# Performance work log

Measured on AMD Instinct MI355X. Metric: run time of the kernel, lower is better.

## Reference

```python
import jax, jax.numpy as jnp
import numpy as np

NUM_CLASSES = 80
CONF_THRE = 0.2
NMS_THRE = 0.45
MAX_DET = 300   # fixed cap replacing torch's variable-length NMS output (padded + keep mask)
IMG = 640.0


def setup_inputs() -> dict:
    key = jax.random.key(0)
    k1, k2 = jax.random.split(key)
    pred = jax.random.uniform(k1, (32, 8400, 85), dtype=jnp.float32)
    # scale cx,cy,w,h to pixel range so IoU/NMS geometry is realistic
    pred = pred.at[..., :4].multiply(IMG)
    zone = jax.random.uniform(k2, (8, 2), dtype=jnp.float32) * IMG
    return {"prediction": pred, "zone": zone}


def _pairwise_iou(b):
    # b: [B, K, 4] in x1y1x2y2
    area = jnp.clip(b[..., 2] - b[..., 0], 0.0) * jnp.clip(b[..., 3] - b[..., 1], 0.0)
    lt = jnp.maximum(b[:, :, None, :2], b[:, None, :, :2])
    rb = jnp.minimum(b[:, :, None, 2:], b[:, None, :, 2:])
    wh = jnp.clip(rb - lt, 0.0)
    inter = wh[..., 0] * wh[..., 1]
    return inter / (area[:, :, None] + area[:, None, :] - inter + 1e-9)


def _postprocess(prediction):
    # decode cx,cy,w,h -> x1,y1,x2,y2
    xy = prediction[..., :2]
    wh = prediction[..., 2:4]
    boxes = jnp.concatenate([xy - wh * 0.5, xy + wh * 0.5], axis=-1)  # [B,N,4]
    obj = prediction[..., 4]                                           # [B,N]
    cls = prediction[..., 5:5 + NUM_CLASSES]
    class_conf = jnp.max(cls, axis=-1)                                 # [B,N]
    class_pred = jnp.argmax(cls, axis=-1)                              # [B,N]

    # confidence mask (obj * class_conf >= thre); invalid -> -inf so top_k drops them
    nms_score = obj * class_conf
    nms_score = jnp.where(nms_score >= CONF_THRE, nms_score, -jnp.inf)

    s, idx = jax.lax.top_k(nms_score, MAX_DET)                         # [B,K]
    b = jnp.take_along_axis(boxes, idx[..., None], axis=1)             # [B,K,4]

    # class-agnostic greedy NMS on score-sorted boxes (matches torchvision.ops.nms)
    iou = _pairwise_iou(b)                                             # [B,K,K]
    keep = jnp.isfinite(s)                                             # valid (passed conf) entries
    ar = jnp.arange(MAX_DET)
    def body(i, keep):
        sup = keep[:, i][:, None] & (iou[:, i, :] > NMS_THRE) & (ar > i)
        return keep & jnp.logical_not(sup)
    keep = jax.lax.fori_loop(0, MAX_DET, body, keep)

    obj_s = jnp.take_along_axis(obj, idx, axis=1)
    conf_s = jnp.take_along_axis(class_conf, idx, axis=1)
    cls_s = jnp.take_along_axis(class_pred, idx, axis=1).astype(jnp.int32)
    # extract_boxes_scores_and_classes: score = max over columns [obj, class_conf]
    scores = jnp.maximum(obj_s, conf_s)
    return b, scores, cls_s, keep


def _points_inside_zone(px, py, zone):
    # px, py: [B,K]; zone: [Z,2]. Ray-casting parity test (faithful to torch version).
    zr = jnp.roll(zone, shift=1, axis=0)
    xi, yi = zone[:, 0], zone[:, 1]
    xj, yj = zr[:, 0], zr[:, 1]
    pyb = py[..., None]  # [B,K,1] vs [Z]
    pxb = px[..., None]
    gyi = yi > pyb
    gyj = yj > pyb
    gx = (xj - xi) * (pyb - yi) / (yj - yi) + xi
    inter = (gyi != gyj) & (gx > pxb)
    return (jnp.sum(inter.astype(jnp.int32), axis=-1) % 2) > 0


def reference(prediction, zone):
    b, scores, classes, keep = _postprocess(prediction)
    cx = (b[..., 0] + b[..., 2]) * 0.5
    cy = (b[..., 1] + b[..., 3]) * 0.5
    in_zone = _points_inside_zone(cx, cy, zone) & keep
    centers_yx = jnp.stack([cy, cx], axis=-1)                          # [B,K,2]
    boxes_yxyx = jnp.stack([b[..., 1], b[..., 0], b[..., 3], b[..., 2]], axis=-1)
    return boxes_yxyx, in_zone, scores, classes, centers_yx, keep
```

## Files before the change

kernel.cpp:

```cpp
#include <hip/hip_runtime.h>
#include <stdint.h>

typedef unsigned long long ull;

#define NA 8400
#define NB 32
#define KTOP 300
#define NC 80
#define CH 33
#define WS_STRIDE 33600
#define OFF_SEL   0
#define OFF_KEEP  2400
#define OFF_MASK  2560

#define O1 38400
#define O2 48000
#define O3 57600
#define O4 67200
#define O5 86400

__global__ __launch_bounds__(256) void score_kernel(const float* __restrict__ pred,
                                                    uint32_t* __restrict__ keys) {
    __shared__ float sP[128 * 85];
    const int blk = blockIdx.x;
    const float4* g4 = (const float4*)(pred + (size_t)blk * 128 * 85);
    float4* l4 = (float4*)sP;
    for (int i = threadIdx.x; i < (128 * 85 / 4); i += 256) l4[i] = g4[i];
    __syncthreads();
    const int t = threadIdx.x;
    if (t < 128) {
        const float* p = sP + t * 85;
        float obj = p[4];
        float b0 = p[5], b1 = p[6], b2 = p[7], b3 = p[8];
        #pragma unroll
        for (int c = 4; c < NC; c += 4) {
            b0 = fmaxf(b0, p[5 + c]);
            b1 = fmaxf(b1, p[6 + c]);
            b2 = fmaxf(b2, p[7 + c]);
            b3 = fmaxf(b3, p[8 + c]);
        }
        float best = fmaxf(fmaxf(b0, b1), fmaxf(b2, b3));
        float sc = obj * best;
        uint32_t u = (sc >= 0.2f) ? (__float_as_uint(sc) | 0x80000000u) : 0x007FFFFFu;
        keys[(size_t)blk * 128 + t] = u;
    }
}

__global__ __launch_bounds__(256) void select_kernel(const uint32_t* keys, uint8_t* ws) {
    __shared__ uint32_t sKeys[8448];
    __shared__ ull sSel[KTOP];
    __shared__ ull sSorted[KTOP];
    __shared__ uint32_t sH4[1024];
    __shared__ uint32_t sScanA[256];
    __shared__ uint32_t sScanB[256];
    __shared__ uint32_t sBc[2];
    __shared__ int sCnt;

    const int b = blockIdx.x;
    const int t = threadIdx.x;
    const int wv = t >> 6;

    for (int e = t; e < NA; e += 256) sKeys[e] = keys[(size_t)b * NA + e];
    for (int e = NA + t; e < 8448; e += 256) sKeys[e] = 0u;
    if (t == 0) sCnt = 0;
    __syncthreads();

    uint32_t prefix = 0, r = KTOP;
    const int beg = t * CH;
    const int end = (beg + CH < NA) ? beg + CH : NA;
    for (int round = 0; round < 4; ++round) {
        const int shift = 24 - 8 * round;
        for (int idx = t; idx < 1024; idx += 256) sH4[idx] = 0u;
        __syncthreads();
        const uint32_t pmask = (round == 0) ? 0u : (0xFFFFFFFFu << (shift + 8));
        for (int e = beg; e < end; ++e) {
            uint32_t k = sKeys[e];
            if ((k & pmask) == (prefix & pmask))
                atomicAdd(&sH4[(wv << 8) + ((k >> shift) & 0xFFu)], 1u);
        }
        __syncthreads();
        sScanA[t] = sH4[t] + sH4[256 + t] + sH4[512 + t] + sH4[768 + t];
        __syncthreads();
        uint32_t* src = sScanA;
        uint32_t* dst = sScanB;
        for (int off = 1; off < 256; off <<= 1) {
            uint32_t v = src[t];
            if (t + off < 256) v += src[t + off];
            dst[t] = v;
            __syncthreads();
            uint32_t* tmp = src; src = dst; dst = tmp;
        }
        uint32_t S = src[t];
        uint32_t above = (t < 255) ? src[t + 1] : 0;
        if (above < r && S >= r) {
            sBc[0] = prefix | ((uint32_t)t << shift);
            sBc[1] = r - above;
        }
        __syncthreads();
        prefix = sBc[0]; r = sBc[1];
        __syncthreads();
    }
    const uint32_t kth = prefix;
    const uint32_t rem = r;
    const uint32_t cntgt = KTOP - rem;

    {
        uint32_t eqc = 0;
        for (int e = beg; e < end; ++e) {
            uint32_t k = sKeys[e];
            if (k > kth) {
                int p = atomicAdd(&sCnt, 1);
                sSel[p] = ((ull)k << 32) | (ull)(0xFFFFFFFFu - (uint32_t)e);
            } else if (k == kth) eqc++;
        }
        sScanA[t] = eqc;
        __syncthreads();
        uint32_t* src = sScanA;
        uint32_t* dst = sScanB;
        for (int off = 1; off < 256; off <<= 1) {
            uint32_t v = src[t];
            if (t >= off) v += src[t - off];
            dst[t] = v;
            __syncthreads();
            uint32_t* tmp = src; src = dst; dst = tmp;
        }
        uint32_t off0 = (t > 0) ? src[t - 1] : 0;
        for (int e = beg; e < end; ++e) {
            uint32_t k = sKeys[e];
            if (k == kth) {
                if (off0 < rem)
                    sSel[cntgt + off0] = ((ull)k << 32) | (ull)(0xFFFFFFFFu - (uint32_t)e);
                off0++;
            }
        }
        __syncthreads();
    }

    ull my0 = sSel[t];
    ull my1 = (t < KTOP - 256) ? sSel[256 + t] : 0ull;
    int r0 = 0, r1 = 0;
    for (int j = 0; j < KTOP; ++j) {
        ull v = sSel[j];
        r0 += (v > my0) ? 1 : 0;
        r1 += (v > my1) ? 1 : 0;
    }
    sSorted[r0] = my0;
    if (t < KTOP - 256) sSorted[r1] = my1;
    __syncthreads();

    ull* selW = (ull*)(ws + (size_t)b * WS_STRIDE + OFF_SEL);
    ull* keepW = (ull*)(ws + (size_t)b * WS_STRIDE + OFF_KEEP);
    bool f = ((uint32_t)(sSorted[t] >> 32)) > 0x007FFFFFu;
    ull m = __ballot(f);
    if ((t & 63) == 0) keepW[t >> 6] = m;
    if (t < 64) {
        bool f2 = (t < KTOP - 256) && (((uint32_t)(sSorted[256 + t] >> 32)) > 0x007FFFFFu);
        ull m2 = __ballot(f2);
        if (t == 0) keepW[4] = m2;
    }
    selW[t] = sSorted[t];
    if (t < KTOP - 256) selW[256 + t] = sSorted[256 + t];
}

__global__ __launch_bounds__(256) void prep_kernel(const float* __restrict__ pred,
                                                   uint8_t* ws,
                                                   float* __restrict__ out) {
    #pragma clang fp contract(off)
    __shared__ float sB0[KTOP], sB1[KTOP], sB2[KTOP], sB3[KTOP];
    const int role = blockIdx.x;
    const int b = blockIdx.y;
    const int t = threadIdx.x;
    const ull* sel = (const ull*)(ws + (size_t)b * WS_STRIDE + OFF_SEL);

    if (role < 5) {
        for (int i = t; i < KTOP; i += 256) {
            uint32_t a = 0xFFFFFFFFu - (uint32_t)sel[i];
            const float* p = pred + ((size_t)b * NA + a) * 85;
            float x = p[0], y = p[1], w = p[2], h = p[3];
            float hw = w * 0.5f, hh = h * 0.5f;
            sB0[i] = x - hw; sB1[i] = y - hh; sB2[i] = x + hw; sB3[i] = y + hh;
        }
        __syncthreads();
        ull* mask = (ull*)(ws + (size_t)b * WS_STRIDE + OFF_MASK);
        const int j0 = role * 64;
        int jmax = j0 + 64; if (jmax > KTOP) jmax = KTOP;
        for (int i = t; i < KTOP; i += 256) {
            float x1 = sB0[i], y1 = sB1[i], x2 = sB2[i], y2 = sB3[i];
            float ai = fmaxf(x2 - x1, 0.0f) * fmaxf(y2 - y1, 0.0f);
            ull bits = 0ull;
            int jbeg = (j0 > i + 1) ? j0 : (i + 1);
            for (int j = jbeg; j < jmax; ++j) {
                float bx1 = sB0[j], by1 = sB1[j], bx2 = sB2[j], by2 = sB3[j];
                float aj = fmaxf(bx2 - bx1, 0.0f) * fmaxf(by2 - by1, 0.0f);
                float iw = fminf(x2, bx2) - fmaxf(x1, bx1); iw = fmaxf(iw, 0.0f);
                float ih = fminf(y2, by2) - fmaxf(y1, by1); ih = fmaxf(ih, 0.0f);
                float inter = iw * ih;
                float den = ai + aj;
                den = den - inter;
                den = den + 1e-9f;
                float iou = inter / den;
                if (iou > 0.45f) bits |= (1ull << (j - j0));
            }
            mask[i * 5 + role] = bits;
        }
    } else {
        const size_t bo = (size_t)b * KTOP;
        for (int i = t; i < KTOP; i += 256) {
            uint32_t a = 0xFFFFFFFFu - (uint32_t)sel[i];
            const float* p = pred + ((size_t)b * NA + a) * 85;
            float x = p[0], y = p[1], w = p[2], h = p[3], obj = p[4];
            float best = p[5]; int bc = 0;
            for (int c = 1; c < NC; ++c) {
                float v = p[5 + c];
                if (v > best) { best = v; bc = c; }
            }
            float hw = w * 0.5f, hh = h * 0.5f;
            float x1 = x - hw, y1 = y - hh, x2 = x + hw, y2 = y + hh;
            out[(bo + i) * 4 + 0] = y1;
            out[(bo + i) * 4 + 1] = x1;
            out[(bo + i) * 4 + 2] = y2;
            out[(bo + i) * 4 + 3] = x2;
            out[O4 + (bo + i) * 2 + 0] = (y1 + y2) * 0.5f;
            out[O4 + (bo + i) * 2 + 1] = (x1 + x2) * 0.5f;
            out[O2 + bo + i] = fmaxf(obj, best);
            out[O3 + bo + i] = (float)bc;
        }
    }
}

__global__ __launch_bounds__(64) void finish_kernel(const float* __restrict__ zone,
                                                    const uint8_t* ws,
                                                    float* __restrict__ out) {
    #pragma clang fp contract(off)
    __shared__ float sZone[16];
    const int b = blockIdx.x;
    const int L = threadIdx.x;
    const ull* mask = (const ull*)(ws + (size_t)b * WS_STRIDE + OFF_MASK);
    const ull* keepI = (const ull*)(ws + (size_t)b * WS_STRIDE + OFF_KEEP);
    if (L < 16) sZone[L] = zone[L];

    ull rm[5][5];
    #pragma unroll
    for (int w = 0; w < 5; ++w) {
        int i = w * 64 + L;
        #pragma unroll
        for (int ww = 0; ww < 5; ++ww)
            rm[w][ww] = (i < KTOP) ? mask[i * 5 + ww] : 0ull;
    }
    ull kw[5];
    #pragma unroll
    for (int w = 0; w < 5; ++w) kw[w] = keepI[w];
    __syncthreads();

    #pragma unroll
    for (int w = 0; w < 5; ++w) {
        ull cur = kw[w];
        while (cur) {
            int ib = __builtin_ctzll(cur);
            ull m0 = __shfl(rm[w][0], ib);
            ull m1 = __shfl(rm[w][1], ib);
            ull m2 = __shfl(rm[w][2], ib);
            ull m3 = __shfl(rm[w][3], ib);
            ull m4 = __shfl(rm[w][4], ib);
            kw[0] &= ~m0; kw[1] &= ~m1; kw[2] &= ~m2; kw[3] &= ~m3; kw[4] &= ~m4;
            ull done = (ib == 63) ? 0ull : (~0ull << (ib + 1));
            cur = kw[w] & done;
        }
    }

    const size_t bo = (size_t)b * KTOP;
    #pragma unroll
    for (int h = 0; h < 5; ++h) {
        int i = h * 64 + L;
        if (i < KTOP) {
            int kp = (int)((kw[h] >> L) & 1ull);
            float cy = out[O4 + (bo + i) * 2 + 0];
            float cx = out[O4 + (bo + i) * 2 + 1];
            int cnt = 0;
            #pragma unroll
            for (int e = 0; e < 8; ++e) {
                float xi = sZone[2 * e], yi = sZone[2 * e + 1];
                int ep = (e + 7) & 7;
                float xj = sZone[2 * ep], yj = sZone[2 * ep + 1];
                bool gyi = yi > cy, gyj = yj > cy;
                if (gyi != gyj) {
                    float gx = (xj - xi) * (cy - yi) / (yj - yi) + xi;
                    if (gx > cx) cnt++;
                }
            }
            int inz = (((cnt & 1) != 0) && kp) ? 1 : 0;
            out[O1 + bo + i] = (float)inz;
            out[O5 + bo + i] = (float)kp;
        }
    }
}

extern "C" void kernel_launch(void* const* d_in, const int* in_sizes, int n_in,
                              void* d_out, int out_size, void* d_ws, size_t ws_size,
                              hipStream_t stream) {
    const float* pred = (const float*)d_in[0];
    const float* zone = (const float*)d_in[1];
    float* out = (float*)d_out;
    uint32_t* keys = (uint32_t*)d_ws;
    uint8_t* ws = (uint8_t*)d_ws;

    score_kernel<<<(NB * NA) / 128, 256, 0, stream>>>(pred, keys);
    select_kernel<<<NB, 256, 0, stream>>>(keys, ws);
    prep_kernel<<<dim3(6, NB), 256, 0, stream>>>(pred, ws, out);
    finish_kernel<<<NB, 64, 0, stream>>>(zone, ws, out);
}
```

Baseline: 203.3 us.

## Fuse select, IoU mask, NMS and zone kernels into one per-batch block

Merges the select, prep and finish kernels into a single per-batch kernel that keeps sorted selections, boxes and the IoU bitmask in a shared-memory union instead of round-tripping through global workspace. It also replaces the block-wide shared-memory scans with wavefront shuffle scans, uses 8 histogram copies instead of 4 to cut atomic contention, and overlaps the serial greedy NMS on wave 0 with output writes on the other waves. The aim is to cut launch overhead, global traffic and barrier count. In exchange, the IoU mask work that ran on 160 blocks now runs on only 32 blocks.

Result: slower. 226.6 us (+11.5%).

```diff
diff --git a/kernel.cpp b/kernel.cpp
--- a/kernel.cpp
+++ b/kernel.cpp
@@ -8,10 +8,6 @@
 #define KTOP 300
 #define NC 80
 #define CH 33
-#define WS_STRIDE 33600
-#define OFF_SEL   0
-#define OFF_KEEP  2400
-#define OFF_MASK  2560
 
 #define O1 38400
 #define O2 48000
@@ -46,22 +42,40 @@
     }
 }
 
-__global__ __launch_bounds__(256) void select_kernel(const uint32_t* keys, uint8_t* ws) {
-    __shared__ uint32_t sKeys[8448];
+__global__ __launch_bounds__(256) void batch_kernel(const float* __restrict__ pred,
+                                                    const float* __restrict__ zone,
+                                                    const uint32_t* __restrict__ keys,
+                                                    float* __restrict__ out) {
+    #pragma clang fp contract(off)
+    __shared__ union {
+        uint32_t keys[8448];
+        struct {
+            float b0[KTOP], b1[KTOP], b2[KTOP], b3[KTOP];
+            ull mask[KTOP * 5];
+        } late;
+    } u;
     __shared__ ull sSel[KTOP];
     __shared__ ull sSorted[KTOP];
-    __shared__ uint32_t sH4[1024];
-    __shared__ uint32_t sScanA[256];
-    __shared__ uint32_t sScanB[256];
+    __shared__ uint32_t sH[8 * 257];
+    __shared__ uint32_t sTot[4];
     __shared__ uint32_t sBc[2];
     __shared__ int sCnt;
+    __shared__ ull sKeepF[5];
+    __shared__ float sZone[16];
 
     const int b = blockIdx.x;
     const int t = threadIdx.x;
+    const int lane = t & 63;
     const int wv = t >> 6;
-
-    for (int e = t; e < NA; e += 256) sKeys[e] = keys[(size_t)b * NA + e];
-    for (int e = NA + t; e < 8448; e += 256) sKeys[e] = 0u;
+    const int hc = t >> 5;
+
+    {
+        const uint4* g4 = (const uint4*)(keys + (size_t)b * NA);
+        uint4* l4 = (uint4*)u.keys;
+        for (int i = t; i < NA / 4; i += 256) l4[i] = g4[i];
+        for (int e = NA + t; e < 8448; e += 256) u.keys[e] = 0u;
+    }
+    if (t < 16) sZone[t] = zone[t];
     if (t == 0) sCnt = 0;
     __syncthreads();
 
@@ -70,35 +84,36 @@
     const int end = (beg + CH < NA) ? beg + CH : NA;
     for (int round = 0; round < 4; ++round) {
         const int shift = 24 - 8 * round;
-        for (int idx = t; idx < 1024; idx += 256) sH4[idx] = 0u;
+        for (int i = t; i < 8 * 257; i += 256) sH[i] = 0u;
         __syncthreads();
         const uint32_t pmask = (round == 0) ? 0u : (0xFFFFFFFFu << (shift + 8));
         for (int e = beg; e < end; ++e) {
-            uint32_t k = sKeys[e];
+            uint32_t k = u.keys[e];
             if ((k & pmask) == (prefix & pmask))
-                atomicAdd(&sH4[(wv << 8) + ((k >> shift) & 0xFFu)], 1u);
-        }
-        __syncthreads();
-        sScanA[t] = sH4[t] + sH4[256 + t] + sH4[512 + t] + sH4[768 + t];
-        __syncthreads();
-        uint32_t* src = sScanA;
-        uint32_t* dst = sScanB;
-        for (int off = 1; off < 256; off <<= 1) {
-            uint32_t v = src[t];
-            if (t + off < 256) v += src[t + off];
-            dst[t] = v;
-            __syncthreads();
-            uint32_t* tmp = src; src = dst; dst = tmp;
-        }
-        uint32_t S = src[t];
-        uint32_t above = (t < 255) ? src[t + 1] : 0;
+                atomicAdd(&sH[hc * 257 + ((k >> shift) & 0xFFu)], 1u);
+        }
+        __syncthreads();
+        uint32_t v = 0;
+        #pragma unroll
+        for (int c = 0; c < 8; ++c) v += sH[c * 257 + t];
+        uint32_t s = v;
+        #pragma unroll
+        for (int off = 1; off < 64; off <<= 1) {
+            uint32_t o = __shfl_down(s, off, 64);
+            if (lane + off < 64) s += o;
+        }
+        if (lane == 0) sTot[wv] = s;
+        __syncthreads();
+        uint32_t S = s;
+        #pragma unroll
+        for (int w2 = 0; w2 < 4; ++w2) if (w2 > wv) S += sTot[w2];
+        uint32_t above = S - v;
         if (above < r && S >= r) {
             sBc[0] = prefix | ((uint32_t)t << shift);
             sBc[1] = r - above;
         }
         __syncthreads();
         prefix = sBc[0]; r = sBc[1];
-        __syncthreads();
     }
     const uint32_t kth = prefix;
     const uint32_t rem = r;
@@ -107,26 +122,25 @@
     {
         uint32_t eqc = 0;
         for (int e = beg; e < end; ++e) {
-            uint32_t k = sKeys[e];
+            uint32_t k = u.keys[e];
             if (k > kth) {
                 int p = atomicAdd(&sCnt, 1);
                 sSel[p] = ((ull)k << 32) | (ull)(0xFFFFFFFFu - (uint32_t)e);
             } else if (k == kth) eqc++;
         }
-        sScanA[t] = eqc;
-        __syncthreads();
-        uint32_t* src = sScanA;
-        uint32_t* dst = sScanB;
-        for (int off = 1; off < 256; off <<= 1) {
-            uint32_t v = src[t];
-            if (t >= off) v += src[t - off];
-            dst[t] = v;
-            __syncthreads();
-            uint32_t* tmp = src; src = dst; dst = tmp;
-        }
-        uint32_t off0 = (t > 0) ? src[t - 1] : 0;
+        uint32_t ps = eqc;
+        #pragma unroll
+        for (int off = 1; off < 64; off <<= 1) {
+            uint32_t o = __shfl_up(ps, off, 64);
+            if (lane >= off) ps += o;
+        }
+        if (lane == 63) sTot[wv] = ps;
+        __syncthreads();
+        uint32_t off0 = ps - eqc;
+        #pragma unroll
+        for (int w2 = 0; w2 < 4; ++w2) if (w2 < wv) off0 += sTot[w2];
         for (int e = beg; e < end; ++e) {
-            uint32_t k = sKeys[e];
+            uint32_t k = u.keys[e];
             if (k == kth) {
                 if (off0 < rem)
                     sSel[cntgt + off0] = ((ull)k << 32) | (ull)(0xFFFFFFFFu - (uint32_t)e);
@@ -136,61 +150,40 @@
         __syncthreads();
     }
 
-    ull my0 = sSel[t];
-    ull my1 = (t < KTOP - 256) ? sSel[256 + t] : 0ull;
-    int r0 = 0, r1 = 0;
-    for (int j = 0; j < KTOP; ++j) {
-        ull v = sSel[j];
-        r0 += (v > my0) ? 1 : 0;
-        r1 += (v > my1) ? 1 : 0;
-    }
-    sSorted[r0] = my0;
-    if (t < KTOP - 256) sSorted[r1] = my1;
-    __syncthreads();
-
-    ull* selW = (ull*)(ws + (size_t)b * WS_STRIDE + OFF_SEL);
-    ull* keepW = (ull*)(ws + (size_t)b * WS_STRIDE + OFF_KEEP);
-    bool f = ((uint32_t)(sSorted[t] >> 32)) > 0x007FFFFFu;
-    ull m = __ballot(f);
-    if ((t & 63) == 0) keepW[t >> 6] = m;
-    if (t < 64) {
-        bool f2 = (t < KTOP - 256) && (((uint32_t)(sSorted[256 + t] >> 32)) > 0x007FFFFFu);
-        ull m2 = __ballot(f2);
-        if (t == 0) keepW[4] = m2;
-    }
-    selW[t] = sSorted[t];
-    if (t < KTOP - 256) selW[256 + t] = sSorted[256 + t];
-}
-
-__global__ __launch_bounds__(256) void prep_kernel(const float* __restrict__ pred,
-                                                   uint8_t* ws,
-                                                   float* __restrict__ out) {
-    #pragma clang fp contract(off)
-    __shared__ float sB0[KTOP], sB1[KTOP], sB2[KTOP], sB3[KTOP];
-    const int role = blockIdx.x;
-    const int b = blockIdx.y;
-    const int t = threadIdx.x;
-    const ull* sel = (const ull*)(ws + (size_t)b * WS_STRIDE + OFF_SEL);
-
-    if (role < 5) {
-        for (int i = t; i < KTOP; i += 256) {
-            uint32_t a = 0xFFFFFFFFu - (uint32_t)sel[i];
-            const float* p = pred + ((size_t)b * NA + a) * 85;
-            float x = p[0], y = p[1], w = p[2], h = p[3];
-            float hw = w * 0.5f, hh = h * 0.5f;
-            sB0[i] = x - hw; sB1[i] = y - hh; sB2[i] = x + hw; sB3[i] = y + hh;
-        }
-        __syncthreads();
-        ull* mask = (ull*)(ws + (size_t)b * WS_STRIDE + OFF_MASK);
+    {
+        ull my0 = sSel[t];
+        ull my1 = (t < KTOP - 256) ? sSel[256 + t] : 0ull;
+        int r0 = 0, r1 = 0;
+        for (int j = 0; j < KTOP; ++j) {
+            ull v = sSel[j];
+            r0 += (v > my0) ? 1 : 0;
+            r1 += (v > my1) ? 1 : 0;
+        }
+        sSorted[r0] = my0;
+        if (t < KTOP - 256) sSorted[r1] = my1;
+        __syncthreads();
+    }
+
+    for (int i = t; i < KTOP; i += 256) {
+        uint32_t a = 0xFFFFFFFFu - (uint32_t)sSorted[i];
+        const float* p = pred + ((size_t)b * NA + a) * 85;
+        float x = p[0], y = p[1], w = p[2], h = p[3];
+        float hw = w * 0.5f, hh = h * 0.5f;
+        u.late.b0[i] = x - hw; u.late.b1[i] = y - hh;
+        u.late.b2[i] = x + hw; u.late.b3[i] = y + hh;
+    }
+    __syncthreads();
+
+    for (int role = 0; role < 5; ++role) {
         const int j0 = role * 64;
         int jmax = j0 + 64; if (jmax > KTOP) jmax = KTOP;
         for (int i = t; i < KTOP; i += 256) {
-            float x1 = sB0[i], y1 = sB1[i], x2 = sB2[i], y2 = sB3[i];
+            float x1 = u.late.b0[i], y1 = u.late.b1[i], x2 = u.late.b2[i], y2 = u.late.b3[i];
             float ai = fmaxf(x2 - x1, 0.0f) * fmaxf(y2 - y1, 0.0f);
             ull bits = 0ull;
             int jbeg = (j0 > i + 1) ? j0 : (i + 1);
             for (int j = jbeg; j < jmax; ++j) {
-                float bx1 = sB0[j], by1 = sB1[j], bx2 = sB2[j], by2 = sB3[j];
+                float bx1 = u.late.b0[j], by1 = u.late.b1[j], bx2 = u.late.b2[j], by2 = u.late.b3[j];
                 float aj = fmaxf(bx2 - bx1, 0.0f) * fmaxf(by2 - by1, 0.0f);
                 float iw = fminf(x2, bx2) - fmaxf(x1, bx1); iw = fmaxf(iw, 0.0f);
                 float ih = fminf(y2, by2) - fmaxf(y1, by1); ih = fmaxf(ih, 0.0f);
@@ -201,12 +194,46 @@
                 float iou = inter / den;
                 if (iou > 0.45f) bits |= (1ull << (j - j0));
             }
-            mask[i * 5 + role] = bits;
+            u.late.mask[i * 5 + role] = bits;
+        }
+    }
+    __syncthreads();
+
+    if (wv == 0) {
+        ull rm[5][5];
+        ull kw[5];
+        #pragma unroll
+        for (int w = 0; w < 5; ++w) {
+            int i = w * 64 + lane;
+            bool f = (i < KTOP) && (((uint32_t)(sSorted[i] >> 32)) > 0x007FFFFFu);
+            kw[w] = __ballot(f);
+            #pragma unroll
+            for (int ww = 0; ww < 5; ++ww)
+                rm[w][ww] = (i < KTOP) ? u.late.mask[i * 5 + ww] : 0ull;
+        }
+        #pragma unroll
+        for (int w = 0; w < 5; ++w) {
+            ull cur = kw[w];
+            while (cur) {
+                int ib = __builtin_ctzll(cur);
+                ull m0 = __shfl(rm[w][0], ib);
+                ull m1 = __shfl(rm[w][1], ib);
+                ull m2 = __shfl(rm[w][2], ib);
+                ull m3 = __shfl(rm[w][3], ib);
+                ull m4 = __shfl(rm[w][4], ib);
+                kw[0] &= ~m0; kw[1] &= ~m1; kw[2] &= ~m2; kw[3] &= ~m3; kw[4] &= ~m4;
+                ull done = (ib == 63) ? 0ull : (~0ull << (ib + 1));
+                cur = kw[w] & done;
+            }
+        }
+        if (lane == 0) {
+            #pragma unroll
+            for (int w = 0; w < 5; ++w) sKeepF[w] = kw[w];
         }
     } else {
         const size_t bo = (size_t)b * KTOP;
-        for (int i = t; i < KTOP; i += 256) {
-            uint32_t a = 0xFFFFFFFFu - (uint32_t)sel[i];
+        for (int i = t - 64; i < KTOP; i += 192) {
+            uint32_t a = 0xFFFFFFFFu - (uint32_t)sSorted[i];
             const float* p = pred + ((size_t)b * NA + a) * 85;
             float x = p[0], y = p[1], w = p[2], h = p[3], obj = p[4];
             float best = p[5]; int bc = 0;
@@ -226,72 +253,28 @@
             out[O3 + bo + i] = (float)bc;
         }
     }
-}
-
-__global__ __launch_bounds__(64) void finish_kernel(const float* __restrict__ zone,
-                                                    const uint8_t* ws,
-                                                    float* __restrict__ out) {
-    #pragma clang fp contract(off)
-    __shared__ float sZone[16];
-    const int b = blockIdx.x;
-    const int L = threadIdx.x;
-    const ull* mask = (const ull*)(ws + (size_t)b * WS_STRIDE + OFF_MASK);
-    const ull* keepI = (const ull*)(ws + (size_t)b * WS_STRIDE + OFF_KEEP);
-    if (L < 16) sZone[L] = zone[L];
-
-    ull rm[5][5];
-    #pragma unroll
-    for (int w = 0; w < 5; ++w) {
-        int i = w * 64 + L;
-        #pragma unroll
-        for (int ww = 0; ww < 5; ++ww)
-            rm[w][ww] = (i < KTOP) ? mask[i * 5 + ww] : 0ull;
-    }
-    ull kw[5];
-    #pragma unroll
-    for (int w = 0; w < 5; ++w) kw[w] = keepI[w];
-    __syncthreads();
-
-    #pragma unroll
-    for (int w = 0; w < 5; ++w) {
-        ull cur = kw[w];
-        while (cur) {
-            int ib = __builtin_ctzll(cur);
-            ull m0 = __shfl(rm[w][0], ib);
-            ull m1 = __shfl(rm[w][1], ib);
-            ull m2 = __shfl(rm[w][2], ib);
-            ull m3 = __shfl(rm[w][3], ib);
-            ull m4 = __shfl(rm[w][4], ib);
-            kw[0] &= ~m0; kw[1] &= ~m1; kw[2] &= ~m2; kw[3] &= ~m3; kw[4] &= ~m4;
-            ull done = (ib == 63) ? 0ull : (~0ull << (ib + 1));
-            cur = kw[w] & done;
-        }
-    }
+    __syncthreads();
 
     const size_t bo = (size_t)b * KTOP;
-    #pragma unroll
-    for (int h = 0; h < 5; ++h) {
-        int i = h * 64 + L;
-        if (i < KTOP) {
-            int kp = (int)((kw[h] >> L) & 1ull);
-            float cy = out[O4 + (bo + i) * 2 + 0];
-            float cx = out[O4 + (bo + i) * 2 + 1];
-            int cnt = 0;
-            #pragma unroll
-            for (int e = 0; e < 8; ++e) {
-                float xi = sZone[2 * e], yi = sZone[2 * e + 1];
-                int ep = (e + 7) & 7;
-                float xj = sZone[2 * ep], yj = sZone[2 * ep + 1];
-                bool gyi = yi > cy, gyj = yj > cy;
-                if (gyi != gyj) {
-                    float gx = (xj - xi) * (cy - yi) / (yj - yi) + xi;
-                    if (gx > cx) cnt++;
-                }
-            }
-            int inz = (((cnt & 1) != 0) && kp) ? 1 : 0;
-            out[O1 + bo + i] = (float)inz;
-            out[O5 + bo + i] = (float)kp;
-        }
+    for (int i = t; i < KTOP; i += 256) {
+        int kp = (int)((sKeepF[i >> 6] >> (i & 63)) & 1ull);
+        float cy = (u.late.b1[i] + u.late.b3[i]) * 0.5f;
+        float cx = (u.late.b0[i] + u.late.b2[i]) * 0.5f;
+        int cnt = 0;
+        #pragma unroll
+        for (int e = 0; e < 8; ++e) {
+            float xi = sZone[2 * e], yi = sZone[2 * e + 1];
+            int ep = (e + 7) & 7;
+            float xj = sZone[2 * ep], yj = sZone[2 * ep + 1];
+            bool gyi = yi > cy, gyj = yj > cy;
+            if (gyi != gyj) {
+                float gx = (xj - xi) * (cy - yi) / (yj - yi) + xi;
+                if (gx > cx) cnt++;
+            }
+        }
+        int inz = (((cnt & 1) != 0) && kp) ? 1 : 0;
+        out[O1 + bo + i] = (float)inz;
+        out[O5 + bo + i] = (float)kp;
     }
 }
 
@@ -302,10 +285,7 @@
     const float* zone = (const float*)d_in[1];
     float* out = (float*)d_out;
     uint32_t* keys = (uint32_t*)d_ws;
-    uint8_t* ws = (uint8_t*)d_ws;
 
     score_kernel<<<(NB * NA) / 128, 256, 0, stream>>>(pred, keys);
-    select_kernel<<<NB, 256, 0, stream>>>(keys, ws);
-    prep_kernel<<<dim3(6, NB), 256, 0, stream>>>(pred, ws, out);
-    finish_kernel<<<NB, 64, 0, stream>>>(zone, ws, out);
+    batch_kernel<<<NB, 256, 0, stream>>>(pred, zone, keys, out);
 }
```
